# Kernel tuning notes

Hardware: AMD Instinct MI355X
Metric: run time of the kernel (lower is better)

## Reference

```python
import jax, jax.numpy as jnp
import numpy as np

N_E = 1024
E_DIM = 64
BETA = 0.25


def setup_inputs() -> dict:
    key = jax.random.key(0)
    k1, k2 = jax.random.split(key)
    z = jax.random.normal(k1, (16, E_DIM, 64, 64), dtype=jnp.float32)
    # torch init: uniform(-1/n_e, 1/n_e)
    emb_w = jax.random.uniform(k2, (N_E, E_DIM), dtype=jnp.float32,
                               minval=-1.0 / N_E, maxval=1.0 / N_E)
    return {"z": z, "emb_w": emb_w}


def reference(z, emb_w):
    bt, ch, h, w = z.shape
    # (B, C, H, W) -> (B, H, W, C) -> (N, e_dim)
    z_perm = jnp.transpose(z, (0, 2, 3, 1))
    z_flat = z_perm.reshape(-1, ch)  # (N, e_dim)

    # squared euclidean distances: (N, n_e)
    distances = (jnp.sum(z_flat ** 2, axis=1, keepdims=True)
                 + jnp.sum(emb_w ** 2, axis=1)
                 - 2.0 * jnp.matmul(z_flat, emb_w.T))
    min_idx = jnp.argmin(distances, axis=1)  # (N,)

    min_encodings = jax.nn.one_hot(min_idx, N_E, dtype=z.dtype)  # (N, n_e)

    # gather codebook vectors (same math as one_hot @ emb_w)
    z_q = emb_w[min_idx].reshape(bt, h, w, ch)
    z_q = jnp.transpose(z_q, (0, 3, 1, 2))  # (B, C, H, W)

    commitment_loss = BETA * jnp.mean((jax.lax.stop_gradient(z_q) - z) ** 2)
    loss = commitment_loss

    # straight-through estimator
    z_q_st = z + jax.lax.stop_gradient(z_q - z)

    avg_probs = jnp.mean(min_encodings, axis=0)
    perplexity = jnp.exp(-jnp.sum(avg_probs * jnp.log(avg_probs + 1e-10)))

    min_encoding_indices = min_idx.reshape(bt, h, w)
    return loss, z_q_st, perplexity, min_encodings, min_encoding_indices
```

## Files before the change

### kernel.cpp

```cpp
#include <hip/hip_runtime.h>
#include <math.h>

#define NPOS   65536
#define NE     1024
#define EDIM   64
#define HW     4096
#define BETA   0.25

#define OUT_LOSS 0LL
#define OUT_ZQ   1LL
#define OUT_PERP 4194305LL
#define OUT_ENC  4194306LL
#define OUT_IDX  71303170LL

__device__ __forceinline__ float pairwise_sum_sq64(const float v[64]) {
#pragma clang fp contract(off)
    float r[8];
#pragma unroll
    for (int k = 0; k < 8; ++k) r[k] = v[k] * v[k];
#pragma unroll
    for (int i = 8; i < 64; i += 8) {
#pragma unroll
        for (int k = 0; k < 8; ++k) {
            float s = v[i + k] * v[i + k];
            r[k] = r[k] + s;
        }
    }
    return ((r[0] + r[1]) + (r[2] + r[3])) + ((r[4] + r[5]) + (r[6] + r[7]));
}

__global__ void vq_prep(const float* __restrict__ emb, float* __restrict__ enorm,
                        float* __restrict__ embT, int* __restrict__ counts,
                        double* __restrict__ lacc) {
    int t = blockIdx.x * 256 + threadIdx.x;
    if (t < NE) {
        float v[64];
#pragma unroll
        for (int c = 0; c < 64; ++c) v[c] = emb[t * 64 + c];
        enorm[t] = pairwise_sum_sq64(v);
#pragma unroll
        for (int c = 0; c < 64; ++c) embT[c * NE + t] = v[c];
        counts[t] = 0;
    }
    if (t == 0) *lacc = 0.0;
}

__global__ __launch_bounds__(256, 4)
void vq_main(const float* __restrict__ z, const float* __restrict__ emb,
             const float* __restrict__ embT, const float* __restrict__ enorm,
             int* __restrict__ counts, double* __restrict__ lacc,
             float* __restrict__ out) {
    __shared__ float dl[256];
    __shared__ int   il[256];
    __shared__ int   fidx[64];

    const int tid = threadIdx.x;
    const int l   = tid & 63;
    const int w   = tid >> 6;
    const int n0  = blockIdx.x * 64;
    const int b   = n0 >> 12;
    const int hw0 = n0 & 4095;
    const int zoff = b * (64 * HW) + hw0 + l;

    float szn;
    {
#pragma clang fp contract(off)
        float r[8];
#pragma unroll
        for (int k = 0; k < 8; ++k) { float x = z[zoff + k * HW]; r[k] = x * x; }
        for (int i = 8; i < 64; i += 8) {
#pragma unroll
            for (int k = 0; k < 8; ++k) {
                float x = z[zoff + (i + k) * HW];
                float s = x * x;
                r[k] = r[k] + s;
            }
        }
        szn = ((r[0] + r[1]) + (r[2] + r[3])) + ((r[4] + r[5]) + (r[6] + r[7]));
    }

    const int jbase = __builtin_amdgcn_readfirstlane(w * 256);

    float best = 3.4e38f;
    int   bi   = jbase;
#pragma clang loop unroll(disable)
    for (int t32 = 0; t32 < 8; ++t32) {
        const int j0 = jbase + t32 * 32;
        float acc[32];
#pragma unroll
        for (int u = 0; u < 32; ++u) acc[u] = 0.0f;

#pragma clang loop unroll_count(4)
        for (int c = 0; c < 64; ++c) {
            const float zc = z[zoff + c * HW];
            const float* __restrict__ er = embT + c * NE + j0;
#pragma unroll
            for (int u = 0; u < 32; ++u) acc[u] = fmaf(zc, er[u], acc[u]);
        }

#pragma unroll
        for (int u = 0; u < 32; ++u) {
            const float dj = (szn + enorm[j0 + u]) - 2.0f * acc[u];
            if (dj < best) { best = dj; bi = j0 + u; }
        }
    }
    dl[tid] = best;
    il[tid] = bi;
    __syncthreads();

    if (w == 0) {
        float bd = dl[l];
        int   bx = il[l];
#pragma unroll
        for (int ww = 1; ww < 4; ++ww) {
            float dw = dl[ww * 64 + l];
            int   iw = il[ww * 64 + l];
            if (dw < bd) { bd = dw; bx = iw; }
        }
        fidx[l] = bx;
        atomicAdd(&counts[bx], 1);
        out[OUT_IDX + n0 + l] = (float)bx;
    }
    __syncthreads();

    {
        float2* __restrict__ enc = (float2*)(out + OUT_ENC);
        const int c0 = tid * 2;
        const int c1 = (tid + 256) * 2;
        for (int r = 0; r < 64; ++r) {
            const int ir = fidx[r];
            const long long rowb = (long long)(n0 + r) * 512;
            float2 v0, v1;
            v0.x = (ir == c0)     ? 1.0f : 0.0f;
            v0.y = (ir == c0 + 1) ? 1.0f : 0.0f;
            v1.x = (ir == c1)     ? 1.0f : 0.0f;
            v1.y = (ir == c1 + 1) ? 1.0f : 0.0f;
            enc[rowb + tid]       = v0;
            enc[rowb + 256 + tid] = v1;
        }
    }

    const int myidx = fidx[l];
    double acc = 0.0;
#pragma unroll
    for (int k = 0; k < 16; ++k) {
        const int c = w * 16 + k;
        const float zc = z[zoff + c * HW];
        const float ec = emb[myidx * 64 + c];
        const float t  = __fsub_rn(ec, zc);
        const float o  = __fadd_rn(zc, t);
        out[OUT_ZQ + (long long)b * (64LL * HW) + (long long)c * HW + hw0 + l] = o;
        const float s = __fmul_rn(t, t);
        acc += (double)s;
    }
#pragma unroll
    for (int off = 32; off > 0; off >>= 1) acc += __shfl_down(acc, off);
    if (l == 0) atomicAdd(lacc, acc);
}

__global__ void vq_finalize(const int* __restrict__ counts,
                            const double* __restrict__ lacc,
                            float* __restrict__ out) {
    __shared__ float red[1024];
    const int t = threadIdx.x;
    const float p = (float)counts[t] * (1.0f / 65536.0f);
    const float term = p * logf(p + 1e-10f);
    red[t] = term;
    __syncthreads();
    for (int s = 512; s > 0; s >>= 1) {
        if (t < s) red[t] += red[t + s];
        __syncthreads();
    }
    if (t == 0) {
        out[OUT_PERP] = expf(-red[0]);
        out[OUT_LOSS] = (float)(BETA * (*lacc / 4194304.0));
    }
}

extern "C" void kernel_launch(void* const* d_in, const int* in_sizes, int n_in,
                              void* d_out, int out_size, void* d_ws, size_t ws_size,
                              hipStream_t stream) {
    const float* z   = (const float*)d_in[0];
    const float* emb = (const float*)d_in[1];
    float* out = (float*)d_out;

    double* lacc  = (double*)d_ws;
    int*    cnts  = (int*)((char*)d_ws + 16);
    float*  enorm = (float*)((char*)d_ws + 16 + NE * sizeof(int));
    float*  embT  = (float*)((char*)d_ws + 16 + NE * sizeof(int) + NE * sizeof(float));

    vq_prep<<<4, 256, 0, stream>>>(emb, enorm, embT, cnts, lacc);
    vq_main<<<1024, 256, 0, stream>>>(z, emb, embT, enorm, cnts, lacc, out);
    vq_finalize<<<1, 1024, 0, stream>>>(cnts, lacc, out);
}
```

Baseline: 197.1 us.

## Tile distance GEMM through LDS with 8x8 register blocking per thread

The distance kernel now stages a 128-position z tile and 128-code embedding tiles in shared memory. Each thread computes an 8x8 outer-product block, where before each thread streamed 32 codes straight from global memory. The argmin is reduced with cross-lane shuffles and a running best per position in LDS, and the z tile is reused for the norm and the straight-through output. This cuts redundant global loads and raises FMA-to-load intensity, at the cost of more LDS (about 70KB), lower occupancy, extra barriers and half as many blocks.

```diff
diff --git a/kernel.cpp b/kernel.cpp
--- a/kernel.cpp
+++ b/kernel.cpp
@@ -12,6 +12,9 @@
 #define OUT_PERP 4194305LL
 #define OUT_ENC  4194306LL
 #define OUT_IDX  71303170LL
+
+#define POSB 128
+#define JT   128
 
 __device__ __forceinline__ float pairwise_sum_sq64(const float v[64]) {
 #pragma clang fp contract(off)
@@ -45,90 +48,128 @@
     if (t == 0) *lacc = 0.0;
 }
 
-__global__ __launch_bounds__(256, 4)
+__global__ __launch_bounds__(256, 2)
 void vq_main(const float* __restrict__ z, const float* __restrict__ emb,
              const float* __restrict__ embT, const float* __restrict__ enorm,
              int* __restrict__ counts, double* __restrict__ lacc,
              float* __restrict__ out) {
-    __shared__ float dl[256];
-    __shared__ int   il[256];
-    __shared__ int   fidx[64];
-
-    const int tid = threadIdx.x;
-    const int l   = tid & 63;
-    const int w   = tid >> 6;
-    const int n0  = blockIdx.x * 64;
-    const int b   = n0 >> 12;
-    const int hw0 = n0 & 4095;
-    const int zoff = b * (64 * HW) + hw0 + l;
-
-    float szn;
-    {
+    __shared__ float z_lds[64 * POSB];
+    __shared__ float e_lds[64 * JT];
+    __shared__ float enorm_lds[NE];
+    __shared__ float szn_lds[POSB];
+    __shared__ float run_d[POSB];
+    __shared__ int   run_j[POSB];
+
+    const int tid   = threadIdx.x;
+    const int tpos  = tid >> 4;
+    const int tcode = tid & 15;
+    const int n0    = blockIdx.x * POSB;
+    const int b     = n0 >> 12;
+    const int hw0   = n0 & 4095;
+    const int zbase = b * (64 * HW) + hw0;
+
+#pragma unroll
+    for (int it = 0; it < 8; ++it) {
+        const int idx4 = it * 256 + tid;
+        const int c    = idx4 >> 5;
+        const int p4   = idx4 & 31;
+        const float4 v = *(const float4*)(z + zbase + c * HW + p4 * 4);
+        *(float4*)(&z_lds[c * POSB + p4 * 4]) = v;
+    }
+#pragma unroll
+    for (int it = 0; it < 4; ++it) enorm_lds[it * 256 + tid] = enorm[it * 256 + tid];
+    if (tid < POSB) { run_d[tid] = 3.4e38f; run_j[tid] = 0; }
+    __syncthreads();
+
+    if (tid < POSB) {
 #pragma clang fp contract(off)
         float r[8];
 #pragma unroll
-        for (int k = 0; k < 8; ++k) { float x = z[zoff + k * HW]; r[k] = x * x; }
+        for (int k = 0; k < 8; ++k) { float x = z_lds[k * POSB + tid]; r[k] = x * x; }
+#pragma unroll
         for (int i = 8; i < 64; i += 8) {
 #pragma unroll
             for (int k = 0; k < 8; ++k) {
-                float x = z[zoff + (i + k) * HW];
+                float x = z_lds[(i + k) * POSB + tid];
                 float s = x * x;
                 r[k] = r[k] + s;
             }
         }
-        szn = ((r[0] + r[1]) + (r[2] + r[3])) + ((r[4] + r[5]) + (r[6] + r[7]));
-    }
-
-    const int jbase = __builtin_amdgcn_readfirstlane(w * 256);
-
-    float best = 3.4e38f;
-    int   bi   = jbase;
-#pragma clang loop unroll(disable)
-    for (int t32 = 0; t32 < 8; ++t32) {
-        const int j0 = jbase + t32 * 32;
-        float acc[32];
-#pragma unroll
-        for (int u = 0; u < 32; ++u) acc[u] = 0.0f;
-
-#pragma clang loop unroll_count(4)
+        szn_lds[tid] = ((r[0] + r[1]) + (r[2] + r[3])) + ((r[4] + r[5]) + (r[6] + r[7]));
+    }
+    __syncthreads();
+
+    for (int jo = 0; jo < 8; ++jo) {
+        const int j0 = jo * JT;
+
+#pragma unroll
+        for (int it = 0; it < 8; ++it) {
+            const int idx4 = it * 256 + tid;
+            const int c    = idx4 >> 5;
+            const int q4   = idx4 & 31;
+            const float4 v = *(const float4*)(embT + c * NE + j0 + q4 * 4);
+            *(float4*)(&e_lds[c * JT + q4 * 4]) = v;
+        }
+        __syncthreads();
+
+        float acc[8][8];
+#pragma unroll
+        for (int i = 0; i < 8; ++i)
+#pragma unroll
+            for (int u = 0; u < 8; ++u) acc[i][u] = 0.0f;
+
+#pragma unroll 2
         for (int c = 0; c < 64; ++c) {
-            const float zc = z[zoff + c * HW];
-            const float* __restrict__ er = embT + c * NE + j0;
-#pragma unroll
-            for (int u = 0; u < 32; ++u) acc[u] = fmaf(zc, er[u], acc[u]);
-        }
-
-#pragma unroll
-        for (int u = 0; u < 32; ++u) {
-            const float dj = (szn + enorm[j0 + u]) - 2.0f * acc[u];
-            if (dj < best) { best = dj; bi = j0 + u; }
-        }
-    }
-    dl[tid] = best;
-    il[tid] = bi;
-    __syncthreads();
-
-    if (w == 0) {
-        float bd = dl[l];
-        int   bx = il[l];
-#pragma unroll
-        for (int ww = 1; ww < 4; ++ww) {
-            float dw = dl[ww * 64 + l];
-            int   iw = il[ww * 64 + l];
-            if (dw < bd) { bd = dw; bx = iw; }
-        }
-        fidx[l] = bx;
-        atomicAdd(&counts[bx], 1);
-        out[OUT_IDX + n0 + l] = (float)bx;
-    }
-    __syncthreads();
+            const float4 za = *(const float4*)(&z_lds[c * POSB + tpos * 8]);
+            const float4 zb = *(const float4*)(&z_lds[c * POSB + tpos * 8 + 4]);
+            const float4 ea = *(const float4*)(&e_lds[c * JT + tcode * 8]);
+            const float4 eb = *(const float4*)(&e_lds[c * JT + tcode * 8 + 4]);
+            const float zf[8] = {za.x, za.y, za.z, za.w, zb.x, zb.y, zb.z, zb.w};
+            const float ef[8] = {ea.x, ea.y, ea.z, ea.w, eb.x, eb.y, eb.z, eb.w};
+#pragma unroll
+            for (int i = 0; i < 8; ++i)
+#pragma unroll
+                for (int u = 0; u < 8; ++u)
+                    acc[i][u] = fmaf(zf[i], ef[u], acc[i][u]);
+        }
+
+#pragma unroll
+        for (int i = 0; i < 8; ++i) {
+            const int p = tpos * 8 + i;
+            const float sz = szn_lds[p];
+            float bd = 3.4e38f;
+            int   bj = 0;
+#pragma unroll
+            for (int u = 0; u < 8; ++u) {
+                const int j = j0 + tcode * 8 + u;
+                const float dj = (sz + enorm_lds[j]) - 2.0f * acc[i][u];
+                if (dj < bd) { bd = dj; bj = j; }
+            }
+#pragma unroll
+            for (int m = 1; m < 16; m <<= 1) {
+                const float od = __shfl_xor(bd, m, 64);
+                const int   oj = __shfl_xor(bj, m, 64);
+                if (od < bd || (od == bd && oj < bj)) { bd = od; bj = oj; }
+            }
+            if (tcode == 0) {
+                if (bd < run_d[p]) { run_d[p] = bd; run_j[p] = bj; }
+            }
+        }
+        __syncthreads();
+    }
+
+    if (tid < POSB) {
+        const int j = run_j[tid];
+        atomicAdd(&counts[j], 1);
+        out[OUT_IDX + n0 + tid] = (float)j;
+    }
 
     {
         float2* __restrict__ enc = (float2*)(out + OUT_ENC);
         const int c0 = tid * 2;
         const int c1 = (tid + 256) * 2;
-        for (int r = 0; r < 64; ++r) {
-            const int ir = fidx[r];
+        for (int r = 0; r < POSB; ++r) {
+            const int ir = run_j[r];
             const long long rowb = (long long)(n0 + r) * 512;
             float2 v0, v1;
             v0.x = (ir == c0)     ? 1.0f : 0.0f;
@@ -140,22 +181,26 @@
         }
     }
 
-    const int myidx = fidx[l];
-    double acc = 0.0;
-#pragma unroll
-    for (int k = 0; k < 16; ++k) {
-        const int c = w * 16 + k;
-        const float zc = z[zoff + c * HW];
-        const float ec = emb[myidx * 64 + c];
-        const float t  = __fsub_rn(ec, zc);
-        const float o  = __fadd_rn(zc, t);
-        out[OUT_ZQ + (long long)b * (64LL * HW) + (long long)c * HW + hw0 + l] = o;
-        const float s = __fmul_rn(t, t);
-        acc += (double)s;
-    }
-#pragma unroll
-    for (int off = 32; off > 0; off >>= 1) acc += __shfl_down(acc, off);
-    if (l == 0) atomicAdd(lacc, acc);
+    {
+        const int pos = tid & 127;
+        const int half = tid >> 7;
+        const int myj = run_j[pos];
+        double acc2 = 0.0;
+#pragma unroll
+        for (int k = 0; k < 32; ++k) {
+            const int c = half * 32 + k;
+            const float zc = z_lds[c * POSB + pos];
+            const float ec = emb[myj * 64 + c];
+            const float t  = __fsub_rn(ec, zc);
+            const float o  = __fadd_rn(zc, t);
+            out[OUT_ZQ + (long long)b * (64LL * HW) + (long long)c * HW + hw0 + pos] = o;
+            const float s = __fmul_rn(t, t);
+            acc2 += (double)s;
+        }
+#pragma unroll
+        for (int off = 32; off > 0; off >>= 1) acc2 += __shfl_down(acc2, off);
+        if ((tid & 63) == 0) atomicAdd(lacc, acc2);
+    }
 }
 
 __global__ void vq_finalize(const int* __restrict__ counts,
@@ -190,6 +235,6 @@
     float*  embT  = (float*)((char*)d_ws + 16 + NE * sizeof(int) + NE * sizeof(float));
 
     vq_prep<<<4, 256, 0, stream>>>(emb, enorm, embT, cnts, lacc);
-    vq_main<<<1024, 256, 0, stream>>>(z, emb, embT, enorm, cnts, lacc, out);
+    vq_main<<<512, 256, 0, stream>>>(z, emb, embT, enorm, cnts, lacc, out);
     vq_finalize<<<1, 1024, 0, stream>>>(cnts, lacc, out);
 }
```

Measured after the change: 195.1 us. About the same (-1.0%).
